# Optimization experiments

Measured on AMD Instinct MI355X. Metric: run time of the kernel, lower is better.

## Reference

```python
import jax, jax.numpy as jnp
import numpy as np

D = 128; H = 4; HD = 32; K = 4; OUT = 2; COND = 6; FF = 256

def _ln(x, g, b):
    m = x.mean(-1, keepdims=True)
    v = ((x - m) ** 2).mean(-1, keepdims=True)
    return g * (x - m) * jax.lax.rsqrt(v + 1e-5) + b

def setup_inputs() -> dict:
    key = jax.random.key(0)
    ks = jax.random.split(key, 40)
    B, S = 4096, 128
    def w(k, shape, scale=0.05):
        return (jax.random.normal(k, shape, dtype=jnp.float32) * scale)
    inp = {
        'x': jax.random.normal(ks[0], (B, OUT, S), dtype=jnp.float32),
        'timesteps': jax.random.randint(ks[1], (B,), 0, 1000, dtype=jnp.int32),
        'conditions': jax.random.normal(ks[2], (B, S, COND), dtype=jnp.float32),
        # time embedding MLP: Linear(128->256), SiLU, Linear(256->128)
        't_w1': w(ks[3], (D, 2 * D)), 't_b1': jnp.zeros((2 * D,), jnp.float32),
        't_w2': w(ks[4], (2 * D, D)), 't_b2': jnp.zeros((D,), jnp.float32),
        # condition MLP: Linear(6->64), SiLU, Linear(64->128), SiLU
        'c_w1': w(ks[5], (COND, D // 2)), 'c_b1': jnp.zeros((D // 2,), jnp.float32),
        'c_w2': w(ks[6], (D // 2, D)), 'c_b2': jnp.zeros((D,), jnp.float32),
        # 2 transformer encoder layers (post-norm, relu FFN, dropout=0 eval)
        'attn_wqkv': w(ks[7], (2, D, 3 * D)), 'attn_bqkv': jnp.zeros((2, 3 * D), jnp.float32),
        'attn_wo': w(ks[8], (2, D, D)), 'attn_bo': jnp.zeros((2, D), jnp.float32),
        'ln1_g': jnp.ones((2, D), jnp.float32), 'ln1_b': jnp.zeros((2, D), jnp.float32),
        'ff_w1': w(ks[9], (2, D, FF)), 'ff_b1': jnp.zeros((2, FF), jnp.float32),
        'ff_w2': w(ks[10], (2, FF, D)), 'ff_b2': jnp.zeros((2, D), jnp.float32),
        'ln2_g': jnp.ones((2, D), jnp.float32), 'ln2_b': jnp.zeros((2, D), jnp.float32),
        # mixture weights net: Linear(256->128), SiLU, Linear(128->4), Softmax
        'mw_w1': w(ks[11], (2 * D, D)), 'mw_b1': jnp.zeros((D,), jnp.float32),
        'mw_w2': w(ks[12], (D, K)), 'mw_b2': jnp.zeros((K,), jnp.float32),
        # K student networks: Linear(2+256->128), Tanh, Linear(128->2)
        's_w1': w(ks[13], (K, OUT + 2 * D, D)), 's_b1': jnp.zeros((K, D), jnp.float32),
        's_w2': w(ks[14], (K, D, OUT)), 's_b2': jnp.zeros((K, OUT), jnp.float32),
    }
    return inp

def reference(x, timesteps, conditions, t_w1, t_b1, t_w2, t_b2, c_w1, c_b1, c_w2, c_b2,
              attn_wqkv, attn_bqkv, attn_wo, attn_bo, ln1_g, ln1_b, ff_w1, ff_b1,
              ff_w2, ff_b2, ln2_g, ln2_b, mw_w1, mw_b1, mw_w2, mw_b2,
              s_w1, s_b1, s_w2, s_b2):
    B, _, S = x.shape
    # sinusoidal time embedding
    half = D // 2
    freqs = jnp.exp(-jnp.log(jnp.float32(10000.0)) * jnp.arange(half, dtype=jnp.float32) / half)
    args = timesteps.astype(jnp.float32)[:, None] * freqs[None, :]
    te = jnp.concatenate([jnp.cos(args), jnp.sin(args)], axis=-1)            # [B, D]
    time_emb = jax.nn.silu(te @ t_w1 + t_b1) @ t_w2 + t_b2                   # [B, D]
    # condition embedding MLP
    h = jax.nn.silu(conditions @ c_w1 + c_b1)
    h = jax.nn.silu(h @ c_w2 + c_b2)                                          # [B, S, D]
    # 2-layer transformer encoder (post-norm)
    for l in range(2):
        qkv = h @ attn_wqkv[l] + attn_bqkv[l]                                 # [B, S, 3D]
        q, k, v = jnp.split(qkv, 3, axis=-1)
        q = q.reshape(B, S, H, HD); k = k.reshape(B, S, H, HD); v = v.reshape(B, S, H, HD)
        sc = jnp.einsum('bqhd,bkhd->bhqk', q, k) / jnp.sqrt(jnp.float32(HD))
        a = jax.nn.softmax(sc, axis=-1)
        o = jnp.einsum('bhqk,bkhd->bqhd', a, v).reshape(B, S, D)
        o = o @ attn_wo[l] + attn_bo[l]
        h = _ln(h + o, ln1_g[l], ln1_b[l])
        f = jax.nn.relu(h @ ff_w1[l] + ff_b1[l]) @ ff_w2[l] + ff_b2[l]
        h = _ln(h + f, ln2_g[l], ln2_b[l])
    cond_emb = h.mean(axis=1)                                                 # [B, D]
    combined = jnp.concatenate([time_emb, cond_emb], axis=-1)                 # [B, 2D]
    mw = jax.nn.softmax(jax.nn.silu(combined @ mw_w1 + mw_b1) @ mw_w2 + mw_b2, axis=-1)  # [B, K]
    # students over all seq positions (vectorized over original seq loop)
    xt = jnp.transpose(x, (0, 2, 1))                                          # [B, S, OUT]
    emb_bs = jnp.broadcast_to(combined[:, None, :], (B, S, 2 * D))
    inp = jnp.concatenate([xt, emb_bs], axis=-1)                              # [B, S, OUT+2D]
    hk = jnp.tanh(jnp.einsum('bsi,kio->bsko', inp, s_w1) + s_b1)              # [B, S, K, D]
    ok = jnp.einsum('bsko,koj->bskj', hk, s_w2) + s_b2                        # [B, S, K, OUT]
    out = jnp.einsum('bskj,bk->bsj', ok, mw)                                  # [B, S, OUT]
    return jnp.transpose(out, (0, 2, 1))                                      # [B, OUT, S]
```

## Files before the change

kernel.cpp:

```cpp
#include <hip/hip_runtime.h>

typedef _Float16 hf;
typedef _Float16 hf2 __attribute__((ext_vector_type(2)));
typedef _Float16 hf4 __attribute__((ext_vector_type(4)));
typedef _Float16 hf8 __attribute__((ext_vector_type(8)));
typedef float f4 __attribute__((ext_vector_type(4)));

#define NTH 512
#define ACT_OFF 0
#define P_OFF   32768
#define SC_OFF  40960
#define SMEM_BYTES 73728

#define WSH_QKV 0
#define WSH_WO  98304
#define WSH_FW1 131072
#define WSH_FW2 196608
#define WSH_CW2 262144
#define WSH_TOTAL 270336
#define CEMB_BYTE_OFF 540672
#define SP1_BYTE_OFF  2637824
#define TPH_SW1 0
#define TPH_TW1 131072
#define TPH_TW2 163840
#define TPH_MW1 196608
#define TPH_TOTAL 229376

__device__ __forceinline__ float dsilu(float x){ return x / (1.f + __expf(-x)); }
__device__ __forceinline__ float dtanh(float x){
  float xc = fminf(fmaxf(x, -10.f), 10.f);
  float e = __expf(2.f * xc);
  return (e - 1.f) / (e + 1.f);
}
__device__ __forceinline__ float fdot2f(hf2 a, hf2 b, float c){
#if __has_builtin(__builtin_amdgcn_fdot2)
  return __builtin_amdgcn_fdot2(a, b, c, false);
#else
  return c + (float)a[0]*(float)b[0] + (float)a[1]*(float)b[1];
#endif
}

__global__ void prep_pack(const float* __restrict__ wqkv, const float* __restrict__ wo,
                          const float* __restrict__ fw1, const float* __restrict__ fw2,
                          const float* __restrict__ cw2, hf* __restrict__ ws){
  int idx = blockIdx.x * 256 + threadIdx.x;
  if (idx >= WSH_TOTAL) return;
  float v;
  if (idx < WSH_WO){
    int u = idx; int lh = u / 12288; int l = lh >> 2, h = lh & 3;
    int r = u % 12288; int tl = r >> 9; int lane = (r >> 3) & 63; int j = r & 7;
    int q = lane >> 4, c = lane & 15;
    int tn = tl >> 2, tk = tl & 3;
    int k = tk*32 + q*8 + j, nloc = tn*16 + c;
    int gcol = (nloc >> 5)*128 + h*32 + (nloc & 31);
    v = wqkv[l*49152 + k*384 + gcol];
  } else if (idx < WSH_FW1){
    int u = idx - WSH_WO; int l = u >> 14; int r = u & 16383;
    int tl = r >> 9; int lane = (r >> 3) & 63; int j = r & 7;
    int q = lane >> 4, c = lane & 15;
    int tn = tl >> 2, tk = tl & 3;
    v = wo[l*16384 + (tk*32 + q*8 + j)*128 + tn*16 + c];
  } else if (idx < WSH_FW2){
    int u = idx - WSH_FW1; int lch = u >> 14; int l = lch >> 1, ch = lch & 1; int r = u & 16383;
    int tl = r >> 9; int lane = (r >> 3) & 63; int j = r & 7;
    int q = lane >> 4, c = lane & 15;
    int tn = tl >> 2, tk = tl & 3;
    v = fw1[l*32768 + (tk*32 + q*8 + j)*256 + ch*128 + tn*16 + c];
  } else if (idx < WSH_CW2){
    int u = idx - WSH_FW2; int lch = u >> 14; int l = lch >> 1, ch = lch & 1; int r = u & 16383;
    int tl = r >> 9; int lane = (r >> 3) & 63; int j = r & 7;
    int q = lane >> 4, c = lane & 15;
    int tn = tl >> 2, tk = tl & 3;
    v = fw2[l*32768 + (ch*128 + tk*32 + q*8 + j)*128 + tn*16 + c];
  } else {
    int u = idx - WSH_CW2;
    int tl = u >> 9; int lane = (u >> 3) & 63; int j = u & 7;
    int q = lane >> 4, c = lane & 15;
    int tn = tl >> 1, tk = tl & 1;
    v = cw2[(tk*32 + q*8 + j)*128 + tn*16 + c];
  }
  ws[idx] = (hf)v;
}

__global__ void prep_pack2(const float* __restrict__ s_w1, const float* __restrict__ t_w1,
                           const float* __restrict__ t_w2, const float* __restrict__ mw_w1,
                           hf* __restrict__ sp1){
  int idx = blockIdx.x * 256 + threadIdx.x;
  if (idx >= TPH_TOTAL) return;
  float v;
  if (idx < TPH_TW1){
    int par = idx & 1, j = (idx >> 1) & 127, ip = (idx >> 8) & 127, k = idx >> 15;
    v = s_w1[k*33024 + (2 + 2*ip + par)*128 + j];
  } else if (idx < TPH_TW2){
    int u = idx - TPH_TW1;
    int par = u & 1, tc = (u >> 1) & 255, ip = u >> 9;
    v = t_w1[(2*ip + par)*256 + tc];
  } else if (idx < TPH_MW1){
    int u = idx - TPH_TW2;
    int par = u & 1, j = (u >> 1) & 127, ip = u >> 8;
    v = t_w2[(2*ip + par)*128 + j];
  } else {
    int u = idx - TPH_MW1;
    int par = u & 1, j = (u >> 1) & 127, ip = u >> 8;
    v = mw_w1[(2*ip + par)*128 + j];
  }
  sp1[idx] = (hf)v;
}

template<int KT>
__device__ __forceinline__ void loadA2(hf8 (&ar)[2][KT], const hf* __restrict__ Ag, int npair, int lane){
#pragma unroll
  for (int jn = 0; jn < 2; ++jn)
#pragma unroll
    for (int tk = 0; tk < KT; ++tk)
      ar[jn][tk] = *(const hf8*)(Ag + (((2*npair + jn)*KT + tk) << 9) + lane*8);
}

template<int KT>
__device__ __forceinline__ void gemmBpre(f4 (&acc)[4][2], const hf8 (&ar)[2][KT], const hf* Bh,
                                         int shalf, int lane){
#pragma unroll
  for (int tk = 0; tk < KT; ++tk){
#pragma unroll
    for (int si = 0; si < 4; ++si){
      hf8 b = *(const hf8*)(Bh + (((shalf*4 + si)*KT + tk) << 9) + lane*8);
      acc[si][0] = __builtin_amdgcn_mfma_f32_16x16x32_f16(ar[0][tk], b, acc[si][0], 0, 0, 0);
      acc[si][1] = __builtin_amdgcn_mfma_f32_16x16x32_f16(ar[1][tk], b, acc[si][1], 0, 0, 0);
    }
  }
}

__device__ __forceinline__ void store_packed_b64(hf* dst, int KtilesOut, int ts, int ft,
                                                 f4 v, int q, int c){
  int tk = ft >> 1;
  int qp = ((ft & 1) << 1) + (q >> 1);
  int j0 = (q & 1) << 2;
  hf4 h; h[0] = (hf)v[0]; h[1] = (hf)v[1]; h[2] = (hf)v[2]; h[3] = (hf)v[3];
  *(hf4*)(dst + ((ts*KtilesOut + tk) << 9) + ((qp*16 + c) << 3) + j0) = h;
}

__device__ __forceinline__ void ln_pass(hf* A, const hf* Dh, const float* __restrict__ g,
                                        const float* __restrict__ bb, int t){
  int s = t >> 2, p = t & 3;
  float xr[4][8];
  int offs[4];
  float sum = 0.f, sq = 0.f;
#pragma unroll
  for (int tk = 0; tk < 4; ++tk){
    int off = (((s >> 4) * 4 + tk) << 9) + ((p * 16 + (s & 15)) << 3);
    offs[tk] = off;
    hf8 va = *(const hf8*)(A + off);
    hf8 vd = *(const hf8*)(Dh + off);
#pragma unroll
    for (int j = 0; j < 8; ++j){
      float x = (float)va[j] + (float)vd[j];
      xr[tk][j] = x; sum += x; sq += x * x;
    }
  }
  sum += __shfl_xor(sum, 1); sq += __shfl_xor(sq, 1);
  sum += __shfl_xor(sum, 2); sq += __shfl_xor(sq, 2);
  float mean = sum * (1.f/128.f);
  float rstd = rsqrtf(sq * (1.f/128.f) - mean*mean + 1e-5f);
#pragma unroll
  for (int tk = 0; tk < 4; ++tk){
    int f0 = tk*32 + p*8;
    f4 g0 = *(const f4*)(g + f0); f4 g1 = *(const f4*)(g + f0 + 4);
    f4 b0 = *(const f4*)(bb + f0); f4 b1 = *(const f4*)(bb + f0 + 4);
    hf8 y;
#pragma unroll
    for (int j = 0; j < 4; ++j){
      y[j]     = (hf)((xr[tk][j]     - mean) * rstd * g0[j] + b0[j]);
      y[j + 4] = (hf)((xr[tk][j + 4] - mean) * rstd * g1[j] + b1[j]);
    }
    *(hf8*)(A + offs[tk]) = y;
  }
}

__global__ __launch_bounds__(NTH, 4) void fused_fp(
    const float* __restrict__ cond,
    const float* __restrict__ c_w1, const float* __restrict__ c_b1, const float* __restrict__ c_b2,
    const float* __restrict__ bqkv_g, const float* __restrict__ bo_g,
    const float* __restrict__ ln1g_g, const float* __restrict__ ln1b_g,
    const float* __restrict__ fb1_g, const float* __restrict__ fb2_g,
    const float* __restrict__ ln2g_g, const float* __restrict__ ln2b_g,
    const hf* __restrict__ wsp, float* __restrict__ cemb)
{
  extern __shared__ char smem[];
  hf* ACTh = (hf*)(smem + ACT_OFF);
  hf* Ph   = (hf*)(smem + P_OFF);
  hf* SCh  = (hf*)(smem + SC_OFF);
  float* SCf = (float*)(smem + SC_OFF);
  hf* Qh  = SCh;
  hf* Kh  = (hf*)(smem + SC_OFF + 8192);
  hf* VTh = (hf*)(smem + SC_OFF + 16384);
  float* cst  = SCf + 4096;
  float* cw1s = SCf + 4864;

  const int b = blockIdx.x;
  const int t = threadIdx.x;
  const int w = t >> 6, lane = t & 63, q = lane >> 4, c = lane & 15;
  const int sp = w & 3, np = w >> 2;
  const int npair = w & 3, shalf = w >> 2;

  for (int idx = t; idx < 768; idx += NTH) cst[idx] = cond[b * 768 + idx];
  if (t < 384) cw1s[t] = c_w1[t];
  if (t < 64)  cw1s[384 + t] = c_b1[t];
  __syncthreads();

  for (int idx = t; idx < 8192; idx += NTH){
    int s = idx >> 6, jf = idx & 63;
    float a = cw1s[384 + jf];
#pragma unroll
    for (int cc = 0; cc < 6; ++cc) a += cst[s * 6 + cc] * cw1s[cc * 64 + jf];
    SCh[(((s >> 4)*2 + (jf >> 5)) << 9) + ((((jf & 31) >> 3)*16 + (s & 15)) << 3) + (jf & 7)] = (hf)dsilu(a);
  }
  {
    hf8 acw[2][2];
    loadA2<2>(acw, wsp + WSH_CW2, npair, lane);
    __syncthreads();
    f4 acc[4][2];
#pragma unroll
    for (int i = 0; i < 4; ++i)
#pragma unroll
      for (int j = 0; j < 2; ++j){ f4 z = {0.f,0.f,0.f,0.f}; acc[i][j] = z; }
    gemmBpre<2>(acc, acw, SCh, shalf, lane);
    f4 cb0 = *(const f4*)(c_b2 + (2*npair    )*16 + q*4);
    f4 cb1 = *(const f4*)(c_b2 + (2*npair + 1)*16 + q*4);
#pragma unroll
    for (int si = 0; si < 4; ++si)
#pragma unroll
      for (int jn = 0; jn < 2; ++jn){
        f4 v = acc[si][jn];
        f4 cb = jn ? cb1 : cb0;
#pragma unroll
        for (int r = 0; r < 4; ++r) v[r] = dsilu(v[r] + cb[r]);
        store_packed_b64(ACTh, 4, shalf*4 + si, 2*npair + jn, v, q, c);
      }
  }

  for (int l = 0; l < 2; ++l){
    f4 oacc[8];
#pragma unroll
    for (int i = 0; i < 8; ++i){ f4 z = {0.f,0.f,0.f,0.f}; oacc[i] = z; }

    for (int h = 0; h < 4; ++h){
      hf8 aq[3][4];
      {
        const hf* Aq = wsp + WSH_QKV + (l*4 + h)*12288;
#pragma unroll
        for (int jn = 0; jn < 3; ++jn)
#pragma unroll
          for (int tk = 0; tk < 4; ++tk)
            aq[jn][tk] = *(const hf8*)(Aq + (((np*3 + jn)*4 + tk) << 9) + lane*8);
      }
      __syncthreads();
      {
        f4 acc[2][3];
#pragma unroll
        for (int i = 0; i < 2; ++i)
#pragma unroll
          for (int j = 0; j < 3; ++j){ f4 z = {0.f,0.f,0.f,0.f}; acc[i][j] = z; }
#pragma unroll
        for (int tk = 0; tk < 4; ++tk){
          hf8 b0 = *(const hf8*)(ACTh + (((2*sp  )*4 + tk) << 9) + lane*8);
          hf8 b1 = *(const hf8*)(ACTh + (((2*sp+1)*4 + tk) << 9) + lane*8);
#pragma unroll
          for (int jn = 0; jn < 3; ++jn){
            acc[0][jn] = __builtin_amdgcn_mfma_f32_16x16x32_f16(aq[jn][tk], b0, acc[0][jn], 0, 0, 0);
            acc[1][jn] = __builtin_amdgcn_mfma_f32_16x16x32_f16(aq[jn][tk], b1, acc[1][jn], 0, 0, 0);
          }
        }
#pragma unroll
        for (int si = 0; si < 2; ++si)
#pragma unroll
          for (int jn = 0; jn < 3; ++jn){
            int ft = np*3 + jn, ts = 2*sp + si;
            int sel = ft >> 1;
            f4 v = acc[si][jn];
            f4 bq = *(const f4*)(bqkv_g + l*384 + sel*128 + h*32 + (ft & 1)*16 + q*4);
#pragma unroll
            for (int r = 0; r < 4; ++r) v[r] += bq[r];
            if (sel == 0){
#pragma unroll
              for (int r = 0; r < 4; ++r) v[r] *= 0.17677669529663687f;
              store_packed_b64(Qh, 1, ts, ft, v, q, c);
            } else if (sel == 1){
              store_packed_b64(Kh, 1, ts, ft - 2, v, q, c);
            } else {
              int td = ft - 4;
              int qp = ((ts & 1) << 1) + (c >> 3);
              hf* pb = VTh + ((td*4 + (ts >> 1)) << 9) + (c & 7);
#pragma unroll
              for (int r = 0; r < 4; ++r) pb[(qp*16 + q*4 + r) << 3] = (hf)v[r];
            }
          }
      }
      __syncthreads();
      {
        hf8 qf = *(const hf8*)(Qh + (w << 9) + lane*8);
        f4 sc[8];
#pragma unroll
        for (int kst = 0; kst < 8; ++kst){
          hf8 kv = *(const hf8*)(Kh + (kst << 9) + lane*8);
          f4 z = {0.f,0.f,0.f,0.f};
          sc[kst] = __builtin_amdgcn_mfma_f32_16x16x32_f16(kv, qf, z, 0, 0, 0);
        }
        float ls = 0.f;
#pragma unroll
        for (int kst = 0; kst < 8; ++kst)
#pragma unroll
          for (int r = 0; r < 4; ++r){
            float e = __expf(sc[kst][r]);
            sc[kst][r] = e; ls += e;
          }
        ls += __shfl_xor(ls, 16);
        ls += __shfl_xor(ls, 32);
        float rl = 1.f / ls;
        hf* Pw = Ph + (w << 9);
#pragma unroll
        for (int ks = 0; ks < 4; ++ks){
#pragma unroll
          for (int h2 = 0; h2 < 2; ++h2){
            int kst = 2*ks + h2;
            int qp = h2*2 + (q >> 1);
            int j0 = (q & 1) << 2;
            hf4 pv;
#pragma unroll
            for (int r = 0; r < 4; ++r) pv[r] = (hf)(sc[kst][r] * rl);
            *(hf4*)(Pw + qp*128 + c*8 + j0) = pv;
          }
          hf8 bp = *(const hf8*)(Pw + lane*8);
          hf8 a0 = *(const hf8*)(VTh + ((     ks) << 9) + lane*8);
          hf8 a1 = *(const hf8*)(VTh + ((4 +  ks) << 9) + lane*8);
          oacc[2*h]     = __builtin_amdgcn_mfma_f32_16x16x32_f16(a0, bp, oacc[2*h],     0, 0, 0);
          oacc[2*h + 1] = __builtin_amdgcn_mfma_f32_16x16x32_f16(a1, bp, oacc[2*h + 1], 0, 0, 0);
        }
      }
    }

    hf8 awo[2][4];
    loadA2<4>(awo, wsp + WSH_WO + l*16384, npair, lane);
    __syncthreads();
#pragma unroll
    for (int ft = 0; ft < 8; ++ft) store_packed_b64(SCh, 4, w, ft, oacc[ft], q, c);
    __syncthreads();

    {
      f4 acc[4][2];
#pragma unroll
      for (int i = 0; i < 4; ++i)
#pragma unroll
        for (int j = 0; j < 2; ++j){ f4 z = {0.f,0.f,0.f,0.f}; acc[i][j] = z; }
      gemmBpre<4>(acc, awo, SCh, shalf, lane);
      __syncthreads();
      f4 bo0 = *(const f4*)(bo_g + l*128 + (2*npair    )*16 + q*4);
      f4 bo1 = *(const f4*)(bo_g + l*128 + (2*npair + 1)*16 + q*4);
#pragma unroll
      for (int si = 0; si < 4; ++si)
#pragma unroll
        for (int jn = 0; jn < 2; ++jn){
          f4 v = acc[si][jn];
          f4 bo = jn ? bo1 : bo0;
#pragma unroll
          for (int r = 0; r < 4; ++r) v[r] += bo[r];
          store_packed_b64(SCh, 4, shalf*4 + si, 2*npair + jn, v, q, c);
        }
    }
    __syncthreads();
    ln_pass(ACTh, SCh, ln1g_g + l*128, ln1b_g + l*128, t);

    {
      f4 facc[4][2];
#pragma unroll
      for (int i = 0; i < 4; ++i)
#pragma unroll
        for (int j = 0; j < 2; ++j){ f4 z = {0.f,0.f,0.f,0.f}; facc[i][j] = z; }
      hf8 af1[2][4], af2[2][4];
      loadA2<4>(af1, wsp + WSH_FW1 + (l*2 + 0)*16384, npair, lane);
      __syncthreads();
      {
        f4 acc[4][2];
#pragma unroll
        for (int i = 0; i < 4; ++i)
#pragma unroll
          for (int j = 0; j < 2; ++j){ f4 z = {0.f,0.f,0.f,0.f}; acc[i][j] = z; }
        gemmBpre<4>(acc, af1, ACTh, shalf, lane);
        f4 fb0 = *(const f4*)(fb1_g + l*256 + (2*npair    )*16 + q*4);
        f4 fb1v = *(const f4*)(fb1_g + l*256 + (2*npair + 1)*16 + q*4);
#pragma unroll
        for (int si = 0; si < 4; ++si)
#pragma unroll
          for (int jn = 0; jn < 2; ++jn){
            f4 v = acc[si][jn];
            f4 fb = jn ? fb1v : fb0;
#pragma unroll
            for (int r = 0; r < 4; ++r) v[r] = fmaxf(v[r] + fb[r], 0.f);
            store_packed_b64(SCh, 4, shalf*4 + si, 2*npair + jn, v, q, c);
          }
      }
      loadA2<4>(af2, wsp + WSH_FW2 + (l*2 + 0)*16384, npair, lane);
      __syncthreads();
      gemmBpre<4>(facc, af2, SCh, shalf, lane);
      loadA2<4>(af1, wsp + WSH_FW1 + (l*2 + 1)*16384, npair, lane);
      __syncthreads();
      {
        f4 acc[4][2];
#pragma unroll
        for (int i = 0; i < 4; ++i)
#pragma unroll
          for (int j = 0; j < 2; ++j){ f4 z = {0.f,0.f,0.f,0.f}; acc[i][j] = z; }
        gemmBpre<4>(acc, af1, ACTh, shalf, lane);
        f4 fb0 = *(const f4*)(fb1_g + l*256 + 128 + (2*npair    )*16 + q*4);
        f4 fb1v = *(const f4*)(fb1_g + l*256 + 128 + (2*npair + 1)*16 + q*4);
#pragma unroll
        for (int si = 0; si < 4; ++si)
#pragma unroll
          for (int jn = 0; jn < 2; ++jn){
            f4 v = acc[si][jn];
            f4 fb = jn ? fb1v : fb0;
#pragma unroll
            for (int r = 0; r < 4; ++r) v[r] = fmaxf(v[r] + fb[r], 0.f);
            store_packed_b64(SCh, 4, shalf*4 + si, 2*npair + jn, v, q, c);
          }
      }
      loadA2<4>(af2, wsp + WSH_FW2 + (l*2 + 1)*16384, npair, lane);
      __syncthreads();
      gemmBpre<4>(facc, af2, SCh, shalf, lane);
      __syncthreads();
      f4 f20 = *(const f4*)(fb2_g + l*128 + (2*npair    )*16 + q*4);
      f4 f21 = *(const f4*)(fb2_g + l*128 + (2*npair + 1)*16 + q*4);
#pragma unroll
      for (int si = 0; si < 4; ++si)
#pragma unroll
        for (int jn = 0; jn < 2; ++jn){
          f4 v = facc[si][jn];
          f4 fb = jn ? f21 : f20;
#pragma unroll
          for (int r = 0; r < 4; ++r) v[r] += fb[r];
          store_packed_b64(SCh, 4, shalf*4 + si, 2*npair + jn, v, q, c);
        }
    }
    __syncthreads();
    ln_pass(ACTh, SCh, ln2g_g + l*128, ln2b_g + l*128, t);
    __syncthreads();
  }

  {
    int o = t & 15;
    float fs[8];
#pragma unroll
    for (int j = 0; j < 8; ++j) fs[j] = 0.f;
#pragma unroll
    for (int u = 0; u < 4; ++u){
      int s = (t >> 4)*4 + u;
      hf8 v = *(const hf8*)(ACTh + (((s >> 4)*4 + (o >> 2)) << 9) + (((o & 3)*16 + (s & 15)) << 3));
#pragma unroll
      for (int j = 0; j < 8; ++j) fs[j] += (float)v[j];
    }
#pragma unroll
    for (int j = 0; j < 8; ++j){
      fs[j] += __shfl_xor(fs[j], 16);
      fs[j] += __shfl_xor(fs[j], 32);
    }
    if (lane < 16){
      f4 v0, v1;
#pragma unroll
      for (int j = 0; j < 4; ++j){ v0[j] = fs[j]; v1[j] = fs[j+4]; }
      *(f4*)(SCf + w*128 + o*8)     = v0;
      *(f4*)(SCf + w*128 + o*8 + 4) = v1;
    }
  }
  __syncthreads();
  if (t < 128){
    float a = 0.f;
#pragma unroll
    for (int wv = 0; wv < 8; ++wv) a += SCf[wv*128 + t];
    cemb[b*128 + t] = a * (1.f/128.f);
  }
}

__global__ __launch_bounds__(256, 8) void tail_k(
    const float* __restrict__ x, const int* __restrict__ tstep, const float* __restrict__ cemb,
    const float* __restrict__ t_b1, const float* __restrict__ t_b2,
    const float* __restrict__ mw_b1,
    const float* __restrict__ mw_w2, const float* __restrict__ mw_b2,
    const float* __restrict__ s_w1, const float* __restrict__ s_b1,
    const float* __restrict__ s_w2, const float* __restrict__ s_b2,
    const hf* __restrict__ sp1, float* __restrict__ out)
{
  __shared__ float sw01[1024], sw2[1024];
  __shared__ float cvec[512];
  __shared__ float scr[1024];
  __shared__ float mwh[128], mwls[4];
  __shared__ hf te_h[128], th_h[256], comb_h[256];
  const int b = blockIdx.x;
  const int t = threadIdx.x;

  for (int i = t; i < 1024; i += 256){
    int row = i >> 9, k = (i >> 7) & 3, j = i & 127;
    sw01[i] = s_w1[k*33024 + row*128 + j];
    sw2[i]  = s_w2[i];
  }
  if (t < 128){
    int i = t & 63;
    float f = __expf(-logf(10000.f) * (float)i * (1.f/64.f));
    float a = (float)tstep[b] * f;
    te_h[t] = (hf)((t < 64) ? cosf(a) : sinf(a));
    comb_h[128 + t] = (hf)cemb[b*128 + t];
  }
  __syncthreads();

  {
    const hf* tp1 = sp1 + TPH_TW1;
    float a = t_b1[t];
#pragma unroll 8
    for (int ii = 0; ii < 64; ++ii){
      hf2 wp = *(const hf2*)(tp1 + ii*512 + 2*t);
      hf2 tp = *(const hf2*)(te_h + 2*ii);
      a = fdot2f(tp, wp, a);
    }
    th_h[t] = (hf)dsilu(a);
  }
  __syncthreads();

  {
    const hf* tp2 = sp1 + TPH_TW2;
    int ih = t >> 7, j = t & 127;
    float a = ih ? 0.f : t_b2[j];
#pragma unroll 8
    for (int ii = 0; ii < 64; ++ii){
      hf2 wp = *(const hf2*)(tp2 + (ih*64 + ii)*256 + 2*j);
      hf2 tp = *(const hf2*)(th_h + ih*128 + 2*ii);
      a = fdot2f(tp, wp, a);
    }
    scr[t] = a;
  }
  __syncthreads();
  if (t < 128) comb_h[t] = (hf)(scr[t] + scr[128 + t]);
  __syncthreads();

  {
    const hf* swp = sp1 + TPH_SW1;
    int ih = t >> 7, k = (t >> 5) & 3, j4 = t & 31;
    f4 a = {0.f, 0.f, 0.f, 0.f};
    const hf* wp = swp + ((k*128 + ih*64)*128 + j4*4)*2;
#pragma unroll 4
    for (int ii = 0; ii < 64; ++ii){
      hf8 wv = *(const hf8*)(wp + ii*256);
      hf2 cb = *(const hf2*)(comb_h + ih*128 + 2*ii);
      hf2 w01; w01[0] = wv[0]; w01[1] = wv[1];
      hf2 w23; w23[0] = wv[2]; w23[1] = wv[3];
      hf2 w45; w45[0] = wv[4]; w45[1] = wv[5];
      hf2 w67; w67[0] = wv[6]; w67[1] = wv[7];
      a[0] = fdot2f(cb, w01, a[0]);
      a[1] = fdot2f(cb, w23, a[1]);
      a[2] = fdot2f(cb, w45, a[2]);
      a[3] = fdot2f(cb, w67, a[3]);
    }
    ((f4*)scr)[ih*128 + k*32 + j4] = a;
  }
  __syncthreads();

  if (t < 128){
    f4 r0 = ((f4*)scr)[t];
    f4 r1 = ((f4*)scr)[128 + t];
    int k = t >> 5, j4 = t & 31;
    f4 sb = *(const f4*)(s_b1 + k*128 + j4*4);
    f4 r; r[0] = r0[0]+r1[0]+sb[0]; r[1] = r0[1]+r1[1]+sb[1];
    r[2] = r0[2]+r1[2]+sb[2]; r[3] = r0[3]+r1[3]+sb[3];
    ((f4*)cvec)[t] = r;
  } else {
    const hf* mp1 = sp1 + TPH_MW1;
    int j = t - 128;
    float a = mw_b1[j];
#pragma unroll 8
    for (int ii = 0; ii < 128; ++ii){
      hf2 wp = *(const hf2*)(mp1 + ii*256 + 2*j);
      hf2 cp = *(const hf2*)(comb_h + 2*ii);
      a = fdot2f(cp, wp, a);
    }
    mwh[j] = dsilu(a);
  }
  __syncthreads();

  if (t < 64){
    int cc = t & 3, j0 = t >> 2;
    float a = 0.f;
#pragma unroll
    for (int i = 0; i < 8; ++i){
      int j = j0 + 16*i;
      a += mwh[j] * mw_w2[j*4 + cc];
    }
    a += __shfl_xor(a, 4);
    a += __shfl_xor(a, 8);
    a += __shfl_xor(a, 16);
    a += __shfl_xor(a, 32);
    if (t < 4) mwls[t] = a + mw_b2[t];
  }
#pragma unroll
  for (int u = 0; u < 2; ++u){
    int o = t + u*256, k = o >> 7, s = o & 127;
    float x0 = x[b*256 + s];
    float x1 = x[b*256 + 128 + s];
    float a0 = 0.f, a1 = 0.f;
    const f4* cvp = (const f4*)cvec + k*32;
    const f4* w0p = (const f4*)sw01 + k*32;
    const f4* w1p = (const f4*)sw01 + 128 + k*32;
    const f4* s2p = (const f4*)sw2 + k*64;
#pragma unroll 2
    for (int j4 = 0; j4 < 32; ++j4){
      f4 cv = cvp[j4], w0 = w0p[j4], w1 = w1p[j4];
      f4 s20 = s2p[2*j4], s21 = s2p[2*j4 + 1];
      float h0 = dtanh(cv[0] + x0*w0[0] + x1*w1[0]);
      float h1 = dtanh(cv[1] + x0*w0[1] + x1*w1[1]);
      float h2 = dtanh(cv[2] + x0*w0[2] + x1*w1[2]);
      float h3 = dtanh(cv[3] + x0*w0[3] + x1*w1[3]);
      a0 += h0*s20[0] + h1*s20[2] + h2*s21[0] + h3*s21[2];
      a1 += h0*s20[1] + h1*s20[3] + h2*s21[1] + h3*s21[3];
    }
    scr[k*256 + s]       = a0 + s_b2[2*k];
    scr[k*256 + 128 + s] = a1 + s_b2[2*k + 1];
  }
  __syncthreads();

  {
    int row = t >> 7, s = t & 127;
    float l0 = mwls[0], l1 = mwls[1], l2 = mwls[2], l3 = mwls[3];
    float mx = fmaxf(fmaxf(l0, l1), fmaxf(l2, l3));
    float e0 = __expf(l0 - mx), e1 = __expf(l1 - mx), e2 = __expf(l2 - mx), e3 = __expf(l3 - mx);
    float rs = 1.f / (e0 + e1 + e2 + e3);
    float a = e0*scr[0*256 + row*128 + s] + e1*scr[1*256 + row*128 + s]
            + e2*scr[2*256 + row*128 + s] + e3*scr[3*256 + row*128 + s];
    out[b*256 + row*128 + s] = a * rs;
  }
}

extern "C" void kernel_launch(void* const* d_in, const int* in_sizes, int n_in,
                              void* d_out, int out_size, void* d_ws, size_t ws_size,
                              hipStream_t stream){
  (void)n_in; (void)ws_size; (void)out_size;
  hipFuncSetAttribute((const void*)fused_fp, hipFuncAttributeMaxDynamicSharedMemorySize, SMEM_BYTES);
  int B = in_sizes[1];
  hf* wsp = (hf*)d_ws;
  float* cemb = (float*)((char*)d_ws + CEMB_BYTE_OFF);
  hf* sp1 = (hf*)((char*)d_ws + SP1_BYTE_OFF);
  prep_pack<<<dim3((WSH_TOTAL + 255) / 256), dim3(256), 0, stream>>>(
      (const float*)d_in[11], (const float*)d_in[13], (const float*)d_in[17],
      (const float*)d_in[19], (const float*)d_in[9], wsp);
  prep_pack2<<<dim3((TPH_TOTAL + 255) / 256), dim3(256), 0, stream>>>(
      (const float*)d_in[27], (const float*)d_in[3], (const float*)d_in[5],
      (const float*)d_in[23], sp1);
  fused_fp<<<dim3(B), dim3(NTH), SMEM_BYTES, stream>>>(
      (const float*)d_in[2],
      (const float*)d_in[7], (const float*)d_in[8], (const float*)d_in[10],
      (const float*)d_in[12], (const float*)d_in[14],
      (const float*)d_in[15], (const float*)d_in[16],
      (const float*)d_in[18], (const float*)d_in[20],
      (const float*)d_in[21], (const float*)d_in[22],
      wsp, cemb);
  tail_k<<<dim3(B), dim3(256), 0, stream>>>(
      (const float*)d_in[0], (const int*)d_in[1], cemb,
      (const float*)d_in[4], (const float*)d_in[6],
      (const float*)d_in[24],
      (const float*)d_in[25], (const float*)d_in[26],
      (const float*)d_in[27], (const float*)d_in[28], (const float*)d_in[29], (const float*)d_in[30],
      sp1, (float*)d_out);
}
```

Measured before the change: 1.053 ms.

## Merge weight-packing kernels, remap layernorm lanes, use fast reciprocal tanh

Combines the two weight-prep kernels into one launch to save a kernel launch. Remaps the layernorm thread-to-row assignment so each wave reads contiguous packed tiles and reduces with xor-16/32 shuffles instead of xor-1/2. Replaces the tanh division with a hardware reciprocal form. The layernorm remap changes which rows threads own, which risks inconsistency with the callers' sync assumptions, and the reciprocal slightly reduces precision.

Result: faster. 973.4 us (-7.5%).

```diff
diff --git a/kernel.cpp b/kernel.cpp
--- a/kernel.cpp
+++ b/kernel.cpp
@@ -30,7 +30,11 @@
 __device__ __forceinline__ float dtanh(float x){
   float xc = fminf(fmaxf(x, -10.f), 10.f);
   float e = __expf(2.f * xc);
+#if __has_builtin(__builtin_amdgcn_rcpf)
+  return 1.f - 2.f * __builtin_amdgcn_rcpf(e + 1.f);
+#else
   return (e - 1.f) / (e + 1.f);
+#endif
 }
 __device__ __forceinline__ float fdot2f(hf2 a, hf2 b, float c){
 #if __has_builtin(__builtin_amdgcn_fdot2)
@@ -40,71 +44,71 @@
 #endif
 }
 
-__global__ void prep_pack(const float* __restrict__ wqkv, const float* __restrict__ wo,
-                          const float* __restrict__ fw1, const float* __restrict__ fw2,
-                          const float* __restrict__ cw2, hf* __restrict__ ws){
+__global__ void prep_all(const float* __restrict__ wqkv, const float* __restrict__ wo,
+                         const float* __restrict__ fw1, const float* __restrict__ fw2,
+                         const float* __restrict__ cw2,
+                         const float* __restrict__ s_w1, const float* __restrict__ t_w1,
+                         const float* __restrict__ t_w2, const float* __restrict__ mw_w1,
+                         hf* __restrict__ ws, hf* __restrict__ sp1){
   int idx = blockIdx.x * 256 + threadIdx.x;
-  if (idx >= WSH_TOTAL) return;
-  float v;
-  if (idx < WSH_WO){
-    int u = idx; int lh = u / 12288; int l = lh >> 2, h = lh & 3;
-    int r = u % 12288; int tl = r >> 9; int lane = (r >> 3) & 63; int j = r & 7;
-    int q = lane >> 4, c = lane & 15;
-    int tn = tl >> 2, tk = tl & 3;
-    int k = tk*32 + q*8 + j, nloc = tn*16 + c;
-    int gcol = (nloc >> 5)*128 + h*32 + (nloc & 31);
-    v = wqkv[l*49152 + k*384 + gcol];
-  } else if (idx < WSH_FW1){
-    int u = idx - WSH_WO; int l = u >> 14; int r = u & 16383;
-    int tl = r >> 9; int lane = (r >> 3) & 63; int j = r & 7;
-    int q = lane >> 4, c = lane & 15;
-    int tn = tl >> 2, tk = tl & 3;
-    v = wo[l*16384 + (tk*32 + q*8 + j)*128 + tn*16 + c];
-  } else if (idx < WSH_FW2){
-    int u = idx - WSH_FW1; int lch = u >> 14; int l = lch >> 1, ch = lch & 1; int r = u & 16383;
-    int tl = r >> 9; int lane = (r >> 3) & 63; int j = r & 7;
-    int q = lane >> 4, c = lane & 15;
-    int tn = tl >> 2, tk = tl & 3;
-    v = fw1[l*32768 + (tk*32 + q*8 + j)*256 + ch*128 + tn*16 + c];
-  } else if (idx < WSH_CW2){
-    int u = idx - WSH_FW2; int lch = u >> 14; int l = lch >> 1, ch = lch & 1; int r = u & 16383;
-    int tl = r >> 9; int lane = (r >> 3) & 63; int j = r & 7;
-    int q = lane >> 4, c = lane & 15;
-    int tn = tl >> 2, tk = tl & 3;
-    v = fw2[l*32768 + (ch*128 + tk*32 + q*8 + j)*128 + tn*16 + c];
+  if (idx < WSH_TOTAL){
+    float v;
+    if (idx < WSH_WO){
+      int u = idx; int lh = u / 12288; int l = lh >> 2, h = lh & 3;
+      int r = u % 12288; int tl = r >> 9; int lane = (r >> 3) & 63; int j = r & 7;
+      int q = lane >> 4, c = lane & 15;
+      int tn = tl >> 2, tk = tl & 3;
+      int k = tk*32 + q*8 + j, nloc = tn*16 + c;
+      int gcol = (nloc >> 5)*128 + h*32 + (nloc & 31);
+      v = wqkv[l*49152 + k*384 + gcol];
+    } else if (idx < WSH_FW1){
+      int u = idx - WSH_WO; int l = u >> 14; int r = u & 16383;
+      int tl = r >> 9; int lane = (r >> 3) & 63; int j = r & 7;
+      int q = lane >> 4, c = lane & 15;
+      int tn = tl >> 2, tk = tl & 3;
+      v = wo[l*16384 + (tk*32 + q*8 + j)*128 + tn*16 + c];
+    } else if (idx < WSH_FW2){
+      int u = idx - WSH_FW1; int lch = u >> 14; int l = lch >> 1, ch = lch & 1; int r = u & 16383;
+      int tl = r >> 9; int lane = (r >> 3) & 63; int j = r & 7;
+      int q = lane >> 4, c = lane & 15;
+      int tn = tl >> 2, tk = tl & 3;
+      v = fw1[l*32768 + (tk*32 + q*8 + j)*256 + ch*128 + tn*16 + c];
+    } else if (idx < WSH_CW2){
+      int u = idx - WSH_FW2; int lch = u >> 14; int l = lch >> 1, ch = lch & 1; int r = u & 16383;
+      int tl = r >> 9; int lane = (r >> 3) & 63; int j = r & 7;
+      int q = lane >> 4, c = lane & 15;
+      int tn = tl >> 2, tk = tl & 3;
+      v = fw2[l*32768 + (ch*128 + tk*32 + q*8 + j)*128 + tn*16 + c];
+    } else {
+      int u = idx - WSH_CW2;
+      int tl = u >> 9; int lane = (u >> 3) & 63; int j = u & 7;
+      int q = lane >> 4, c = lane & 15;
+      int tn = tl >> 1, tk = tl & 1;
+      v = cw2[(tk*32 + q*8 + j)*128 + tn*16 + c];
+    }
+    ws[idx] = (hf)v;
   } else {
-    int u = idx - WSH_CW2;
-    int tl = u >> 9; int lane = (u >> 3) & 63; int j = u & 7;
-    int q = lane >> 4, c = lane & 15;
-    int tn = tl >> 1, tk = tl & 1;
-    v = cw2[(tk*32 + q*8 + j)*128 + tn*16 + c];
-  }
-  ws[idx] = (hf)v;
-}
-
-__global__ void prep_pack2(const float* __restrict__ s_w1, const float* __restrict__ t_w1,
-                           const float* __restrict__ t_w2, const float* __restrict__ mw_w1,
-                           hf* __restrict__ sp1){
-  int idx = blockIdx.x * 256 + threadIdx.x;
-  if (idx >= TPH_TOTAL) return;
-  float v;
-  if (idx < TPH_TW1){
-    int par = idx & 1, j = (idx >> 1) & 127, ip = (idx >> 8) & 127, k = idx >> 15;
-    v = s_w1[k*33024 + (2 + 2*ip + par)*128 + j];
-  } else if (idx < TPH_TW2){
-    int u = idx - TPH_TW1;
-    int par = u & 1, tc = (u >> 1) & 255, ip = u >> 9;
-    v = t_w1[(2*ip + par)*256 + tc];
-  } else if (idx < TPH_MW1){
-    int u = idx - TPH_TW2;
-    int par = u & 1, j = (u >> 1) & 127, ip = u >> 8;
-    v = t_w2[(2*ip + par)*128 + j];
-  } else {
-    int u = idx - TPH_MW1;
-    int par = u & 1, j = (u >> 1) & 127, ip = u >> 8;
-    v = mw_w1[(2*ip + par)*128 + j];
-  }
-  sp1[idx] = (hf)v;
+    int ix = idx - WSH_TOTAL;
+    if (ix >= TPH_TOTAL) return;
+    float v;
+    if (ix < TPH_TW1){
+      int par = ix & 1, j = (ix >> 1) & 127, ip = (ix >> 8) & 127, k = ix >> 15;
+      v = s_w1[k*33024 + (2 + 2*ip + par)*128 + j];
+    } else if (ix < TPH_TW2){
+      int u = ix - TPH_TW1;
+      int par = u & 1, tc = (u >> 1) & 255, ip = u >> 9;
+      v = t_w1[(2*ip + par)*256 + tc];
+    } else if (ix < TPH_MW1){
+      int u = ix - TPH_TW2;
+      int par = u & 1, j = (u >> 1) & 127, ip = u >> 8;
+      v = t_w2[(2*ip + par)*128 + j];
+    } else {
+      int u = ix - TPH_MW1;
+      int par = u & 1, j = (u >> 1) & 127, ip = u >> 8;
+      v = mw_w1[(2*ip + par)*128 + j];
+    }
+    sp1[ix] = (hf)v;
+  }
 }
 
 template<int KT>
@@ -141,13 +145,13 @@
 
 __device__ __forceinline__ void ln_pass(hf* A, const hf* Dh, const float* __restrict__ g,
                                         const float* __restrict__ bb, int t){
-  int s = t >> 2, p = t & 3;
+  int w = t >> 6, lane = t & 63, qp = lane >> 4;
   float xr[4][8];
   int offs[4];
   float sum = 0.f, sq = 0.f;
 #pragma unroll
   for (int tk = 0; tk < 4; ++tk){
-    int off = (((s >> 4) * 4 + tk) << 9) + ((p * 16 + (s & 15)) << 3);
+    int off = ((w*4 + tk) << 9) + lane*8;
     offs[tk] = off;
     hf8 va = *(const hf8*)(A + off);
     hf8 vd = *(const hf8*)(Dh + off);
@@ -157,13 +161,13 @@
       xr[tk][j] = x; sum += x; sq += x * x;
     }
   }
-  sum += __shfl_xor(sum, 1); sq += __shfl_xor(sq, 1);
-  sum += __shfl_xor(sum, 2); sq += __shfl_xor(sq, 2);
+  sum += __shfl_xor(sum, 16); sq += __shfl_xor(sq, 16);
+  sum += __shfl_xor(sum, 32); sq += __shfl_xor(sq, 32);
   float mean = sum * (1.f/128.f);
   float rstd = rsqrtf(sq * (1.f/128.f) - mean*mean + 1e-5f);
 #pragma unroll
   for (int tk = 0; tk < 4; ++tk){
-    int f0 = tk*32 + p*8;
+    int f0 = tk*32 + qp*8;
     f4 g0 = *(const f4*)(g + f0); f4 g1 = *(const f4*)(g + f0 + 4);
     f4 b0 = *(const f4*)(bb + f0); f4 b1 = *(const f4*)(bb + f0 + 4);
     hf8 y;
@@ -644,12 +648,11 @@
   hf* wsp = (hf*)d_ws;
   float* cemb = (float*)((char*)d_ws + CEMB_BYTE_OFF);
   hf* sp1 = (hf*)((char*)d_ws + SP1_BYTE_OFF);
-  prep_pack<<<dim3((WSH_TOTAL + 255) / 256), dim3(256), 0, stream>>>(
+  prep_all<<<dim3((WSH_TOTAL + TPH_TOTAL + 255) / 256), dim3(256), 0, stream>>>(
       (const float*)d_in[11], (const float*)d_in[13], (const float*)d_in[17],
-      (const float*)d_in[19], (const float*)d_in[9], wsp);
-  prep_pack2<<<dim3((TPH_TOTAL + 255) / 256), dim3(256), 0, stream>>>(
+      (const float*)d_in[19], (const float*)d_in[9],
       (const float*)d_in[27], (const float*)d_in[3], (const float*)d_in[5],
-      (const float*)d_in[23], sp1);
+      (const float*)d_in[23], wsp, sp1);
   fused_fp<<<dim3(B), dim3(NTH), SMEM_BYTES, stream>>>(
       (const float*)d_in[2],
       (const float*)d_in[7], (const float*)d_in[8], (const float*)d_in[10],
```
